# Kernel optimization log

Hardware: AMD Instinct MI355X
Metric: run time of the kernel (lower is better)

## Reference

```python
import jax, jax.numpy as jnp
import numpy as np

B, DIM, IN_DIM, H, W = 4, 256, 128, 128, 128
DD = IN_DIM // 2          # down_dim = 64
HEADS = 8
BN_EPS = 1e-5


def conv2d(x, w, b=None, pad=0, dil=1):
    y = jax.lax.conv_general_dilated(
        x, w, window_strides=(1, 1),
        padding=[(pad, pad), (pad, pad)],
        rhs_dilation=(dil, dil),
        dimension_numbers=('NCHW', 'OIHW', 'NCHW'))
    if b is not None:
        y = y + b[None, :, None, None]
    return y


def bn_relu(x, s, o):
    # eval-mode BatchNorm2d with running_mean=0, running_var=1
    return jax.nn.relu(x * (s / np.sqrt(1.0 + BN_EPS))[None, :, None, None] + o[None, :, None, None])


def setup_inputs() -> dict:
    ks = iter(jax.random.split(jax.random.key(0), 80))

    def w(shape, sc=0.05):
        return sc * jax.random.normal(next(ks), shape, jnp.float32)

    def s(c):
        return 1.0 + 0.1 * jax.random.normal(next(ks), (c,), jnp.float32)

    def o(c):
        return 0.02 * jax.random.normal(next(ks), (c,), jnp.float32)

    d = {}
    d['x'] = jax.random.normal(next(ks), (B, DIM, H, W), jnp.float32)
    d['w_dc'] = w((IN_DIM, DIM, 3, 3)); d['b_dc'] = w((IN_DIM,)); d['s_dc'] = s(IN_DIM); d['o_dc'] = o(IN_DIM)
    d['w1'] = w((DD, IN_DIM, 1, 1)); d['b1'] = w((DD,)); d['s1'] = s(DD); d['o1'] = o(DD)
    d['w2'] = w((DD, DD, 3, 3)); d['b2'] = w((DD,)); d['s2'] = s(DD); d['o2'] = o(DD)
    d['w3'] = w((DD, DD, 3, 3)); d['b3'] = w((DD,)); d['s3'] = s(DD); d['o3'] = o(DD)
    d['w4'] = w((DD, DD, 3, 3)); d['b4'] = w((DD,)); d['s4'] = s(DD); d['o4'] = o(DD)
    d['w5'] = w((DD, IN_DIM, 1, 1)); d['b5'] = w((DD,)); d['s5'] = s(DD); d['o5'] = o(DD)
    d['temperature'] = jnp.ones((HEADS, 1, 1), jnp.float32)
    d['w_po'] = w((DD, 2 * DD, 1, 1))  # project_out, bias=False
    d['w_wa'] = w((DD // 16, DD, 1, 1)); d['b_wa'] = w((DD // 16,)); d['s_wa'] = s(DD // 16); d['o_wa'] = o(DD // 16)
    d['w_wb'] = w((DD, DD // 16, 1, 1)); d['b_wb'] = w((DD,))
    d['w_f'] = w((DD, 5 * DD, 1, 1)); d['b_f'] = w((DD,)); d['s_f'] = s(DD); d['o_f'] = o(DD)
    d['w_oa'] = w((DD // 2, DD, 3, 3)); d['b_oa'] = w((DD // 2,)); d['s_oa'] = s(DD // 2); d['o_oa'] = o(DD // 2)
    d['w_ob'] = w((1, DD // 2, 1, 1)); d['b_ob'] = w((1,))
    return d


def reference(x, w_dc, b_dc, s_dc, o_dc, w1, b1, s1, o1, w2, b2, s2, o2,
              w3, b3, s3, o3, w4, b4, s4, o4, w5, b5, s5, o5,
              temperature, w_po, w_wa, b_wa, s_wa, o_wa, w_wb, b_wb,
              w_f, b_f, s_f, o_f, w_oa, b_oa, s_oa, o_oa, w_ob, b_ob):

    def branch(c):
        b, ch, h, wd = c.shape
        f = jnp.fft.fft2(c)                                   # [b,ch,h,w] complex64 (q=k=v=tepqkv)
        qkv = f.reshape(b, HEADS, ch // HEADS, h * wd)        # v (unnormalized)
        n = jnp.sqrt(jnp.sum(jnp.square(jnp.abs(qkv)), axis=-1, keepdims=True))
        qn = qkv / jnp.maximum(n, 1e-12)                      # F.normalize(dim=-1); q == k
        attn = jnp.einsum('bhcn,bhdn->bhcd', qn, qn) * temperature
        # custom complex normalization: separate real/imag softmax
        attn = jax.lax.complex(jax.nn.softmax(attn.real, axis=-1),
                               jax.nn.softmax(attn.imag, axis=-1))
        of = jnp.abs(jnp.fft.ifft2(jnp.einsum('bhcd,bhdn->bhcn', attn, qkv)))  # ifft2 over (c, hw)
        of = of.reshape(b, ch, h, wd)
        g = jax.nn.sigmoid(conv2d(bn_relu(conv2d(f.real, w_wa, b_wa), s_wa, o_wa), w_wb, b_wb))
        ol = jnp.abs(jnp.fft.ifft2(g * f))                    # ifft2 over (h, w)
        return conv2d(jnp.concatenate([of, ol], axis=1), w_po) + c

    xd = bn_relu(conv2d(x, w_dc, b_dc, pad=1), s_dc, o_dc)
    c1 = bn_relu(conv2d(xd, w1, b1), s1, o1)
    c2 = bn_relu(conv2d(c1, w2, b2, pad=3, dil=3), s2, o2)
    F2 = branch(c2)
    c3 = bn_relu(conv2d(c1 + F2, w3, b3, pad=5, dil=5), s3, o3)
    F3 = branch(c3)
    c4 = bn_relu(conv2d(c1 + F3, w4, b4, pad=7, dil=7), s4, o4)
    F4 = branch(c4)
    # conv5: global avg pool -> 1x1 conv -> bilinear upsample of a 1x1 map == broadcast
    c5 = bn_relu(conv2d(jnp.mean(xd, axis=(2, 3), keepdims=True), w5, b5), s5, o5)
    c5 = jnp.broadcast_to(c5, (c5.shape[0], c5.shape[1], xd.shape[2], xd.shape[3]))
    fused = bn_relu(conv2d(jnp.concatenate([c1, F2, F3, F4, c5], axis=1), w_f, b_f), s_f, o_f)
    return conv2d(bn_relu(conv2d(fused, w_oa, b_oa, pad=1), s_oa, o_oa), w_ob, b_ob)
```

## Files before the change

### kernel.cpp

```cpp
#include <hip/hip_runtime.h>

#define S 16384
#define PI_F 3.14159265358979f

struct Ptrs { const float* p[43]; };

enum : int {
  O_SBDC=0, O_SB1=256, O_SB2=512, O_SB3=768, O_SB4=1024, O_SB5=1280,
  O_SBWA=1536, O_SBF=1792, O_SBOA=2048,
  O_M=2304, O_C5=2816, O_NRM=3072, O_GRAM=3328, O_ATT2=7424, O_BEFF=11520,
  O_WB=16384,
  O_PART=147456,
  O_H=180224,
  O_WP=442368,
  O_A=524288,
  O_FIN=8912896,
  O_CC=25690112,
  O_DRE=29884416, O_DIMG=34078720,
  O_ERE=38273024, O_EIM=42467328,
  O_G=46661632
};

typedef short bfrag __attribute__((ext_vector_type(8)));
typedef float ffrag __attribute__((ext_vector_type(4)));

__device__ __forceinline__ float bf2f(unsigned short u){
  union { unsigned int i; float f; } v; v.i = ((unsigned int)u) << 16; return v.f;
}
__device__ __forceinline__ unsigned short f2bf(float f){
  unsigned int x = __float_as_uint(f);
  unsigned int r = x + 0x7fffu + ((x >> 16) & 1u);
  return (unsigned short)(r >> 16);
}

__global__ void prep_sb_kernel(Ptrs P, float* ws){
  const float r = rsqrtf(1.0f + 1e-5f);
  int bi=0, si=0, oi=0, C=0, dst=0;
  switch (blockIdx.x){
    case 0: bi=2; si=3; oi=4; C=128; dst=O_SBDC; break;
    case 1: bi=6; si=7; oi=8; C=64; dst=O_SB1; break;
    case 2: bi=10; si=11; oi=12; C=64; dst=O_SB2; break;
    case 3: bi=14; si=15; oi=16; C=64; dst=O_SB3; break;
    case 4: bi=18; si=19; oi=20; C=64; dst=O_SB4; break;
    case 5: bi=22; si=23; oi=24; C=64; dst=O_SB5; break;
    case 6: bi=28; si=29; oi=30; C=4;  dst=O_SBWA; break;
    case 7: bi=34; si=35; oi=36; C=64; dst=O_SBF; break;
    default: bi=38; si=39; oi=40; C=32; dst=O_SBOA; break;
  }
  for (int c = threadIdx.x; c < C; c += 256){
    float bb = P.p[bi][c], ss = P.p[si][c], oo = P.p[oi][c];
    float sc = ss * r;
    ws[dst + c] = sc;
    ws[dst + C + c] = bb * sc + oo;
  }
}

__global__ __launch_bounds__(256) void xpad_kernel(const float* __restrict__ x,
    unsigned short* __restrict__ XT){
  int yy = blockIdx.x, b = blockIdx.y;
  long obase = ((long)(b*130) + yy) * (130L*256);
  int tid = threadIdx.x;
  if (yy == 0 || yy == 129){
    uint4 z; z.x=0; z.y=0; z.z=0; z.w=0;
    for (int i = tid; i < 130*256/8; i += 256)
      *(uint4*)(XT + obase + (long)i*8) = z;
    return;
  }
  __shared__ float LT[64][129];
  int y = yy - 1;
  for (int c0 = 0; c0 < 256; c0 += 64){
    for (int idx = tid; idx < 64*128; idx += 256){
      int ci = idx >> 7, xx = idx & 127;
      LT[ci][xx] = x[((long)(b*256 + c0 + ci)*128 + y)*128 + xx];
    }
    __syncthreads();
    for (int idx = tid; idx < 128*16; idx += 256){
      int xp = idx >> 4, c4 = (idx & 15)*4;
      ushort4 v;
      v.x = f2bf(LT[c4][xp]);   v.y = f2bf(LT[c4+1][xp]);
      v.z = f2bf(LT[c4+2][xp]); v.w = f2bf(LT[c4+3][xp]);
      *(ushort4*)(XT + obase + (long)(xp+1)*256 + c0 + c4) = v;
    }
    __syncthreads();
  }
  if (tid < 64){
    ushort4 z; z.x=0; z.y=0; z.z=0; z.w=0;
    *(ushort4*)(XT + obase + tid*4) = z;
    *(ushort4*)(XT + obase + 129L*256 + tid*4) = z;
  }
}

__global__ void wt_kernel(const float* __restrict__ w, unsigned short* __restrict__ WH,
    unsigned short* __restrict__ WL){
  for (int e = blockIdx.x*256 + threadIdx.x; e < 294912; e += gridDim.x*256){
    int c32 = e & 31, co = (e >> 5) & 127, kc = (e >> 12) & 7, sh = e >> 15;
    int ky = sh / 3, kx = sh - ky*3;
    int ci = kc*32 + c32;
    float v = w[((long)(co*256 + ci)*3 + ky)*3 + kx];
    unsigned short h = f2bf(v);
    WH[e] = h;
    WL[e] = f2bf(v - bf2f(h));
  }
}

__global__ void wtg_kernel(Ptrs P, unsigned short* __restrict__ WB){
  const float* w; int cout; long off;
  switch (blockIdx.y){
    case 0: w = P.p[9];  cout = 64; off = 0;      break;
    case 1: w = P.p[13]; cout = 64; off = 73728;  break;
    case 2: w = P.p[17]; cout = 64; off = 147456; break;
    default: w = P.p[37]; cout = 32; off = 221184; break;
  }
  int total = 576*cout;
  unsigned short* WH = WB + off;
  unsigned short* WL = WH + total;
  for (int e = blockIdx.x*256 + threadIdx.x; e < total; e += gridDim.x*256){
    int c32 = e & 31;
    int co = (e >> 5) & (cout - 1);
    int kc = (e / (32*cout)) & 1;
    int sh = e / (64*cout);
    int ky = sh/3, kx = sh - ky*3;
    int ci = kc*32 + c32;
    float v = w[((long)(co*64 + ci)*3 + ky)*3 + kx];
    unsigned short h = f2bf(v);
    WH[e] = h;
    WL[e] = f2bf(v - bf2f(h));
  }
}

__global__ void wtp_kernel(Ptrs P, unsigned short* __restrict__ WP){
  const float* w; int KC, wstr; long off;
  switch (blockIdx.y){
    case 0: w = P.p[5];  KC = 4; wstr = 128; off = 0;     break;
    case 1: w = P.p[26]; KC = 4; wstr = 128; off = 16384; break;
    default: w = P.p[33]; KC = 8; wstr = 320; off = 32768; break;
  }
  int total = KC*64*32;
  unsigned short* WH = WP + off;
  unsigned short* WL = WH + total;
  for (int e = blockIdx.x*256 + threadIdx.x; e < total; e += gridDim.x*256){
    int c32 = e & 31, co = (e >> 5) & 63, kc = e >> 11;
    float v = w[(long)co*wstr + kc*32 + c32];
    unsigned short h = f2bf(v);
    WH[e] = h;
    WL[e] = f2bf(v - bf2f(h));
  }
}

template<int DIL, int BF16IN>
__global__ __launch_bounds__(256) void xpad64_kernel(const void* __restrict__ in1,
    const void* __restrict__ in2, long in_bs, unsigned short* __restrict__ XP){
  constexpr int TW = 128 + 2*DIL;
  int yy = blockIdx.x, b = blockIdx.y;
  long obase = (long)(b*TW + yy) * TW * 64;
  int tid = threadIdx.x;
  if (yy < DIL || yy >= 128 + DIL){
    uint4 z; z.x=0; z.y=0; z.z=0; z.w=0;
    for (int i = tid; i < TW*8; i += 256)
      *(uint4*)(XP + obase + (long)i*8) = z;
    return;
  }
  __shared__ float LT[64][129];
  int y = yy - DIL;
  if (BF16IN){
    const unsigned short* p1 = (const unsigned short*)in1 + (long)b*in_bs + (long)y*128;
    const unsigned short* p2 = in2 ? (const unsigned short*)in2 + (long)b*in_bs + (long)y*128 : nullptr;
    for (int idx = tid; idx < 64*64; idx += 256){
      int ci = idx >> 6, x2 = (idx & 63)*2;
      ushort2 u1 = *(const ushort2*)(p1 + (long)ci*S + x2);
      float a0 = bf2f(u1.x), a1 = bf2f(u1.y);
      if (p2){
        ushort2 u2 = *(const ushort2*)(p2 + (long)ci*S + x2);
        a0 += bf2f(u2.x); a1 += bf2f(u2.y);
      }
      LT[ci][x2] = a0; LT[ci][x2+1] = a1;
    }
  } else {
    const float* p1 = (const float*)in1 + (long)b*in_bs + (long)y*128;
    for (int idx = tid; idx < 64*128; idx += 256){
      int ci = idx >> 7, xx = idx & 127;
      LT[ci][xx] = p1[(long)ci*S + xx];
    }
  }
  __syncthreads();
  for (int i = tid; i < 2*DIL*16; i += 256){
    int side = i / (DIL*16);
    int r = i - side*(DIL*16);
    int xcol = side ? (128 + DIL + (r >> 4)) : (r >> 4);
    ushort4 z; z.x=0; z.y=0; z.z=0; z.w=0;
    *(ushort4*)(XP + obase + (long)xcol*64 + (r & 15)*4) = z;
  }
  for (int idx = tid; idx < 128*16; idx += 256){
    int xp = idx >> 4, c4 = (idx & 15)*4;
    ushort4 v;
    v.x = f2bf(LT[c4][xp]);   v.y = f2bf(LT[c4+1][xp]);
    v.z = f2bf(LT[c4+2][xp]); v.w = f2bf(LT[c4+3][xp]);
    *(ushort4*)(XP + obase + (long)(xp + DIL)*64 + c4) = v;
  }
}

template<int DIL, int KC, int NBLK, int BF16OUT>
__global__ __launch_bounds__(256) void conv3x3_mfma_kernel(
    const unsigned short* __restrict__ XP,
    const unsigned short* __restrict__ WH, const unsigned short* __restrict__ WL,
    const float* __restrict__ scbi, void* __restrict__ out){
  constexpr int CIN = KC*32;
  constexpr int TW = 128 + 2*DIL;
  constexpr int NJ = NBLK/32;
  constexpr int LDA = 36;
  constexpr int NSTG = (TW + 63)/64;
  constexpr int NS = 3*KC;
  __shared__ unsigned short As[2][TW*LDA];
  int bid = blockIdx.x;
  int y = (bid & 7)*16 + ((bid >> 3) & 15);
  int b = (bid >> 7) & 3;
  int n2 = bid >> 9;
  int nb = gridDim.x >> 9; if (nb == 0) nb = 1;
  int coutTotal = nb * NBLK;
  int tid = threadIdx.x, wv = tid >> 6, lane = tid & 63;
  int mhalf = wv & 1, nhalf = wv >> 1;
  int px0 = mhalf*64;
  ffrag acc[4][NJ];
  #pragma unroll
  for (int i = 0; i < 4; i++)
    #pragma unroll
    for (int j = 0; j < NJ; j++)
      #pragma unroll
      for (int r = 0; r < 4; r++) acc[i][j][r] = 0.f;

  int kq = (lane >> 4)*8, rown = lane & 15;
  int sx = tid >> 2, sq = tid & 3;
  int cobase = n2*NBLK + nhalf*(NBLK/2);

  {
    long rowbase = ((long)(b*TW + y))*TW*CIN + sq*8;
    #pragma unroll
    for (int t = 0; t < NSTG; t++){
      int x = sx + 64*t;
      int xc = x < TW ? x : TW - 1;
      uint4 v = *(const uint4*)(XP + rowbase + (long)xc*CIN);
      if (x < TW) *(uint4*)&As[0][x*LDA + sq*8] = v;
    }
  }
  __syncthreads();

  for (int s = 0; s < NS; s++){
    int cur = s & 1;
    int ky = s / KC, kc = s - ky*KC;
    int s2 = (s + 1 < NS) ? s + 1 : s;
    int ky2 = s2 / KC, kc2 = s2 - ky2*KC;
    uint4 pre[NSTG];
    {
      long rowbase = ((long)(b*TW + y + ky2*DIL))*TW*CIN + kc2*32 + sq*8;
      #pragma unroll
      for (int t = 0; t < NSTG; t++){
        int x = sx + 64*t;
        int xc = x < TW ? x : TW - 1;
        pre[t] = *(const uint4*)(XP + rowbase + (long)xc*CIN);
      }
    }
    #pragma unroll
    for (int kx = 0; kx < 3; kx++){
      int step = (ky*3 + kx)*KC + kc;
      bfrag bhf[NJ], blf[NJ];
      #pragma unroll
      for (int j = 0; j < NJ; j++){
        long wb = ((long)step*coutTotal + cobase + j*16 + rown)*32 + kq;
        bhf[j] = *(const bfrag*)(WH + wb);
        blf[j] = *(const bfrag*)(WL + wb);
      }
      bfrag af[4];
      #pragma unroll
      for (int i = 0; i < 4; i++){
        int x = px0 + i*16 + rown + kx*DIL;
        af[i] = *(const bfrag*)&As[cur][x*LDA + kq];
      }
      #pragma unroll
      for (int i = 0; i < 4; i++)
        #pragma unroll
        for (int j = 0; j < NJ; j++){
          acc[i][j] = __builtin_amdgcn_mfma_f32_16x16x32_bf16(af[i], blf[j], acc[i][j], 0, 0, 0);
          acc[i][j] = __builtin_amdgcn_mfma_f32_16x16x32_bf16(af[i], bhf[j], acc[i][j], 0, 0, 0);
        }
    }
    #pragma unroll
    for (int t = 0; t < NSTG; t++){
      int x = sx + 64*t;
      if (x < TW) *(uint4*)&As[cur ^ 1][x*LDA + sq*8] = pre[t];
    }
    __syncthreads();
  }
  #pragma unroll
  for (int i = 0; i < 4; i++){
    int pixel = px0 + i*16 + (lane >> 4)*4;
    #pragma unroll
    for (int j = 0; j < NJ; j++){
      int co = cobase + j*16 + (lane & 15);
      float sc = scbi[co], bb = scbi[coutTotal + co];
      long ooff = ((long)(b*coutTotal + co))*S + y*128 + pixel;
      if (BF16OUT){
        ushort4 w;
        w.x = f2bf(fmaxf(acc[i][j][0]*sc + bb, 0.f));
        w.y = f2bf(fmaxf(acc[i][j][1]*sc + bb, 0.f));
        w.z = f2bf(fmaxf(acc[i][j][2]*sc + bb, 0.f));
        w.w = f2bf(fmaxf(acc[i][j][3]*sc + bb, 0.f));
        *(ushort4*)((unsigned short*)out + ooff) = w;
      } else {
        float* op = (float*)out + ooff;
        #pragma unroll
        for (int r = 0; r < 4; r++)
          op[r] = fmaxf(acc[i][j][r]*sc + bb, 0.f);
      }
    }
  }
}

template<int MODE, int KC, int BF16IN, int BF16OUT>
__global__ __launch_bounds__(256) void conv1x1_mfma_kernel(
    const void* __restrict__ inv, long in_bs,
    const unsigned short* __restrict__ WH, const unsigned short* __restrict__ WL,
    const float* __restrict__ scbi, const float* __restrict__ beff,
    const unsigned short* __restrict__ res, long res_bs,
    void* __restrict__ outv, long out_bs){
  constexpr int LDA = 36;
  __shared__ unsigned short Als[128*LDA];
  __shared__ unsigned short BHs[64*LDA];
  __shared__ unsigned short BLs[64*LDA];
  int bid = blockIdx.x;
  int y = (bid & 7)*16 + ((bid >> 3) & 15);
  int b = bid >> 7;
  int tid = threadIdx.x, wv = tid >> 6, lane = tid & 63;
  int mt0 = (wv & 1)*4, nt0 = (wv >> 1)*2;
  ffrag acc[4][2];
  #pragma unroll
  for (int i = 0; i < 4; i++)
    #pragma unroll
    for (int j = 0; j < 2; j++)
      #pragma unroll
      for (int r = 0; r < 4; r++) acc[i][j][r] = 0.f;
  int pq = tid & 31, cg = tid >> 5;
  int kq = (lane >> 4)*8, rown = lane & 15;
  int wrB = (tid >> 2)*LDA + (tid & 3)*8;
  const float* ibf = (const float*)inv + (long)b*in_bs + y*128;
  const unsigned short* ibs = (const unsigned short*)inv + (long)b*in_bs + y*128;
  unsigned short a[16];
  uint4 BHr, BLr;
  #pragma unroll
  for (int cc = 0; cc < 4; cc++)
    #pragma unroll
    for (int i = 0; i < 4; i++){
      if (BF16IN) a[cc*4 + i] = ibs[(long)(cg*4 + cc)*S + pq + 32*i];
      else        a[cc*4 + i] = f2bf(ibf[(long)(cg*4 + cc)*S + pq + 32*i]);
    }
  BHr = *(const uint4*)(WH + tid*8);
  BLr = *(const uint4*)(WL + tid*8);
  for (int kc = 0; kc < KC; kc++){
    __syncthreads();
    #pragma unroll
    for (int i = 0; i < 4; i++){
      ushort4 v;
      v.x = a[0 + i];  v.y = a[4 + i];
      v.z = a[8 + i];  v.w = a[12 + i];
      *(ushort4*)&Als[(pq + 32*i)*LDA + cg*4] = v;
    }
    *(uint4*)&BHs[wrB] = BHr;
    *(uint4*)&BLs[wrB] = BLr;
    __syncthreads();
    if (kc + 1 < KC){
      #pragma unroll
      for (int cc = 0; cc < 4; cc++)
        #pragma unroll
        for (int i = 0; i < 4; i++){
          long off = (long)((kc + 1)*32 + cg*4 + cc)*S + pq + 32*i;
          if (BF16IN) a[cc*4 + i] = ibs[off];
          else        a[cc*4 + i] = f2bf(ibf[off]);
        }
      long gw = (long)(kc + 1)*2048;
      BHr = *(const uint4*)(WH + gw + tid*8);
      BLr = *(const uint4*)(WL + gw + tid*8);
    }
    bfrag af[4], bhf[2], blf[2];
    #pragma unroll
    for (int i = 0; i < 4; i++)
      af[i] = *(const bfrag*)&Als[((mt0 + i)*16 + rown)*LDA + kq];
    #pragma unroll
    for (int j = 0; j < 2; j++){
      bhf[j] = *(const bfrag*)&BHs[((nt0 + j)*16 + rown)*LDA + kq];
      blf[j] = *(const bfrag*)&BLs[((nt0 + j)*16 + rown)*LDA + kq];
    }
    #pragma unroll
    for (int i = 0; i < 4; i++)
      #pragma unroll
      for (int j = 0; j < 2; j++){
        acc[i][j] = __builtin_amdgcn_mfma_f32_16x16x32_bf16(af[i], blf[j], acc[i][j], 0, 0, 0);
        acc[i][j] = __builtin_amdgcn_mfma_f32_16x16x32_bf16(af[i], bhf[j], acc[i][j], 0, 0, 0);
      }
  }
  #pragma unroll
  for (int i = 0; i < 4; i++){
    int pixel = (mt0 + i)*16 + (lane >> 4)*4;
    #pragma unroll
    for (int j = 0; j < 2; j++){
      int co = (nt0 + j)*16 + (lane & 15);
      long ooff = (long)b*out_bs + (long)co*S + y*128 + pixel;
      float vv[4];
      if (MODE == 1){
        ushort4 rv = *(const ushort4*)(res + (long)b*res_bs + (long)co*S + y*128 + pixel);
        vv[0] = acc[i][j][0] + bf2f(rv.x);
        vv[1] = acc[i][j][1] + bf2f(rv.y);
        vv[2] = acc[i][j][2] + bf2f(rv.z);
        vv[3] = acc[i][j][3] + bf2f(rv.w);
      } else if (MODE == 0){
        #pragma unroll
        for (int r = 0; r < 4; r++)
          vv[r] = fmaxf(acc[i][j][r]*scbi[co] + scbi[64 + co], 0.f);
      } else {
        #pragma unroll
        for (int r = 0; r < 4; r++)
          vv[r] = fmaxf(acc[i][j][r]*scbi[co] + beff[b*64 + co], 0.f);
      }
      if (BF16OUT){
        ushort4 w;
        w.x = f2bf(vv[0]); w.y = f2bf(vv[1]); w.z = f2bf(vv[2]); w.w = f2bf(vv[3]);
        *(ushort4*)((unsigned short*)outv + ooff) = w;
      } else {
        float* op = (float*)outv + ooff;
        #pragma unroll
        for (int r = 0; r < 4; r++) op[r] = vv[r];
      }
    }
  }
}

__device__ __forceinline__ void fft128_mk_tw(float (&tws)[8], float (&twc)[8],
                                             float sign, int lane){
  float a0 = sign * (2.0f*PI_F/128.0f) * (float)lane;
  __sincosf(a0, &tws[0], &twc[0]);
  int i = 1;
  #pragma unroll
  for (int h = 32; h >= 1; h >>= 1, i++){
    int j = lane & (h - 1);
    float a = sign * (2.0f*PI_F/128.0f) * (float)(j * (64/h));
    __sincosf(a, &tws[i], &twc[i]);
  }
}

__device__ __forceinline__ void fft128(float& z0r, float& z0i, float& z1r, float& z1i,
    const float (&tws)[8], const float (&twc)[8], int lane){
  {
    float ar = z0r, ai = z0i, br = z1r, bi = z1i;
    z0r = ar + br; z0i = ai + bi;
    float dr = ar - br, di = ai - bi;
    float s = tws[0], c = twc[0];
    z1r = dr*c - di*s; z1i = dr*s + di*c;
  }
  int idx = 1;
  #pragma unroll
  for (int h = 32; h >= 1; h >>= 1, idx++){
    float s = tws[idx], c = twc[idx];
    bool up = (lane & h) != 0;
    float pr, pi, nr, ni;
    pr = __shfl_xor(z0r, h, 64); pi = __shfl_xor(z0i, h, 64);
    if (!up){ nr = z0r + pr; ni = z0i + pi; }
    else { float dr = pr - z0r, di = pi - z0i; nr = dr*c - di*s; ni = dr*s + di*c; }
    z0r = nr; z0i = ni;
    pr = __shfl_xor(z1r, h, 64); pi = __shfl_xor(z1i, h, 64);
    if (!up){ nr = z1r + pr; ni = z1i + pi; }
    else { float dr = pr - z1r, di = pi - z1i; nr = dr*c - di*s; ni = dr*s + di*c; }
    z1r = nr; z1i = ni;
  }
}


__global__ __launch_bounds__(1024) void fft2_fwd_kernel(const unsigned short* __restrict__ in,
    unsigned short* __restrict__ outRe, unsigned short* __restrict__ outIm){
  __shared__ float lre[128][129];
  __shared__ float lim[128][129];
  int plane = blockIdx.x;
  int tid = threadIdx.x, wv = tid >> 6, lane = tid & 63;
  long pbase = (long)plane * S;
  for (int i = tid; i < S/4; i += 1024){
    int px = i*4; int r = px >> 7, c = px & 127;
    ushort4 v = *(const ushort4*)(in + pbase + px);
    lre[r][c] = bf2f(v.x); lre[r][c+1] = bf2f(v.y);
    lre[r][c+2] = bf2f(v.z); lre[r][c+3] = bf2f(v.w);
  }
  float tws[8], twc[8];
  fft128_mk_tw(tws, twc, -1.0f, lane);
  __syncthreads();
  #pragma unroll
  for (int rr = 0; rr < 8; rr++){
    int r = wv*8 + rr;
    float z0r = lre[r][lane], z0i = 0.f;
    float z1r = lre[r][lane + 64], z1i = 0.f;
    fft128(z0r, z0i, z1r, z1i, tws, twc, lane);
    int k = __brev(lane) >> 25;
    lre[r][k] = z0r;     lim[r][k] = z0i;
    lre[r][k+1] = z1r;   lim[r][k+1] = z1i;
  }
  __syncthreads();
  #pragma unroll
  for (int cc = 0; cc < 8; cc++){
    int c = wv*8 + cc;
    float z0r = lre[lane][c], z0i = lim[lane][c];
    float z1r = lre[lane + 64][c], z1i = lim[lane + 64][c];
    fft128(z0r, z0i, z1r, z1i, tws, twc, lane);
    int k = __brev(lane) >> 25;
    lre[k][c] = z0r;     lim[k][c] = z0i;
    lre[k+1][c] = z1r;   lim[k+1][c] = z1i;
  }
  __syncthreads();
  for (int i = tid; i < S/2; i += 1024){
    int px = i*2; int r = px >> 7, c = px & 127;
    ushort2 vr, vi;
    vr.x = f2bf(lre[r][c]); vr.y = f2bf(lre[r][c+1]);
    vi.x = f2bf(lim[r][c]); vi.y = f2bf(lim[r][c+1]);
    *(ushort2*)(outRe + pbase + px) = vr;
    *(ushort2*)(outIm + pbase + px) = vi;
  }
}

__global__ __launch_bounds__(1024) void ifft2_gate_abs_ol_kernel(
    const unsigned short* __restrict__ Dre, const unsigned short* __restrict__ Dim,
    const float* __restrict__ H, const float* __restrict__ wb, const float* __restrict__ bwb,
    unsigned short* __restrict__ AB){
  __shared__ float lre[128][129];
  __shared__ float lim[128][129];
  int plane = blockIdx.x;
  int b = plane >> 6, ch = plane & 63;
  int tid = threadIdx.x, wv = tid >> 6, lane = tid & 63;
  long pbase = (long)plane * S;
  float w0 = wb[ch*4], w1 = wb[ch*4+1], w2 = wb[ch*4+2], w3 = wb[ch*4+3];
  float bw = bwb[ch];
  const float* Hb = H + (long)b*4*S;
  for (int i = tid; i < S/2; i += 1024){
    int px = i*2;
    float2 h0 = *(const float2*)(Hb + px);
    float2 h1 = *(const float2*)(Hb + S + px);
    float2 h2 = *(const float2*)(Hb + 2*S + px);
    float2 h3 = *(const float2*)(Hb + 3*S + px);
    ushort2 ur = *(const ushort2*)(Dre + pbase + px);
    ushort2 ui = *(const ushort2*)(Dim + pbase + px);
    float hva = bw + w0*h0.x + w1*h1.x + w2*h2.x + w3*h3.x;
    float hvb = bw + w0*h0.y + w1*h1.y + w2*h2.y + w3*h3.y;
    float ga = 1.0f / (1.0f + __expf(-hva));
    float gb = 1.0f / (1.0f + __expf(-hvb));
    int r = px >> 7, c = px & 127;
    lre[r][c]   = bf2f(ur.x) * ga;  lim[r][c]   = bf2f(ui.x) * ga;
    lre[r][c+1] = bf2f(ur.y) * gb;  lim[r][c+1] = bf2f(ui.y) * gb;
  }
  float tws[8], twc[8];
  fft128_mk_tw(tws, twc, 1.0f, lane);
  __syncthreads();
  #pragma unroll
  for (int cc = 0; cc < 8; cc++){
    int c = wv*8 + cc;
    float z0r = lre[lane][c], z0i = lim[lane][c];
    float z1r = lre[lane + 64][c], z1i = lim[lane + 64][c];
    fft128(z0r, z0i, z1r, z1i, tws, twc, lane);
    int k = __brev(lane) >> 25;
    lre[k][c] = z0r;     lim[k][c] = z0i;
    lre[k+1][c] = z1r;   lim[k+1][c] = z1i;
  }
  __syncthreads();
  unsigned short* out = AB + ((long)(b*128 + 64 + ch)) * S;
  #pragma unroll
  for (int rr = 0; rr < 8; rr++){
    int r = wv*8 + rr;
    float z0r = lre[r][lane], z0i = lim[r][lane];
    float z1r = lre[r][lane + 64], z1i = lim[r][lane + 64];
    fft128(z0r, z0i, z1r, z1i, tws, twc, lane);
    int k = __brev(lane) >> 25;
    ushort2 v;
    v.x = f2bf(sqrtf(z0r*z0r + z0i*z0i) * (1.0f/16384.0f));
    v.y = f2bf(sqrtf(z1r*z1r + z1i*z1i) * (1.0f/16384.0f));
    *(ushort2*)(out + (long)r*128 + k) = v;
  }
}

__global__ __launch_bounds__(1024) void ifft2_attn_abs_ofT_kernel(
    const unsigned short* __restrict__ Dre, const unsigned short* __restrict__ Dim,
    const float* __restrict__ ATT2, unsigned short* __restrict__ AB){
  __shared__ float lre[128][129];
  __shared__ float lim[128][129];
  int plane = blockIdx.x;
  int b = plane >> 6, ch = plane & 63;
  int bh = plane >> 3;
  int cp = plane & 7;
  int tid = threadIdx.x, wv = tid >> 6, lane = tid & 63;
  long hbase = (long)bh * 8 * S;
  float wr[8], wi[8];
  #pragma unroll
  for (int d = 0; d < 8; d++){
    wr[d] = ATT2[bh*128 + (cp*8 + d)*2];
    wi[d] = ATT2[bh*128 + (cp*8 + d)*2 + 1];
  }
  for (int i = tid; i < S/4; i += 1024){
    int px = i*4;
    float sr0=0.f, si0=0.f, sr1=0.f, si1=0.f, sr2=0.f, si2=0.f, sr3=0.f, si3=0.f;
    #pragma unroll
    for (int d = 0; d < 8; d++){
      ushort4 ur = *(const ushort4*)(Dre + hbase + (long)d*S + px);
      ushort4 ui = *(const ushort4*)(Dim + hbase + (long)d*S + px);
      float xr0 = bf2f(ur.x), xi0 = bf2f(ui.x);
      float xr1 = bf2f(ur.y), xi1 = bf2f(ui.y);
      float xr2 = bf2f(ur.z), xi2 = bf2f(ui.z);
      float xr3 = bf2f(ur.w), xi3 = bf2f(ui.w);
      sr0 += wr[d]*xr0 - wi[d]*xi0;  si0 += wr[d]*xi0 + wi[d]*xr0;
      sr1 += wr[d]*xr1 - wi[d]*xi1;  si1 += wr[d]*xi1 + wi[d]*xr1;
      sr2 += wr[d]*xr2 - wi[d]*xi2;  si2 += wr[d]*xi2 + wi[d]*xr2;
      sr3 += wr[d]*xr3 - wi[d]*xi3;  si3 += wr[d]*xi3 + wi[d]*xr3;
    }
    int r = px >> 7, c = px & 127;
    lre[r][c]   = sr0;  lim[r][c]   = si0;
    lre[r][c+1] = sr1;  lim[r][c+1] = si1;
    lre[r][c+2] = sr2;  lim[r][c+2] = si2;
    lre[r][c+3] = sr3;  lim[r][c+3] = si3;
  }
  float tws[8], twc[8];
  fft128_mk_tw(tws, twc, 1.0f, lane);
  __syncthreads();
  #pragma unroll
  for (int cc = 0; cc < 8; cc++){
    int c = wv*8 + cc;
    float z0r = lre[lane][c], z0i = lim[lane][c];
    float z1r = lre[lane + 64][c], z1i = lim[lane + 64][c];
    fft128(z0r, z0i, z1r, z1i, tws, twc, lane);
    int k = __brev(lane) >> 25;
    float s, co;
    float a0 = (2.0f*PI_F/16384.0f) * (float)(c * k);
    __sincosf(a0, &s, &co);
    float t = z0r*co - z0i*s; z0i = z0r*s + z0i*co; z0r = t;
    float a1 = (2.0f*PI_F/16384.0f) * (float)(c * (k + 1));
    __sincosf(a1, &s, &co);
    t = z1r*co - z1i*s; z1i = z1r*s + z1i*co; z1r = t;
    lre[k][c] = z0r;     lim[k][c] = z0i;
    lre[k+1][c] = z1r;   lim[k+1][c] = z1i;
  }
  __syncthreads();
  float absv[8][2];
  #pragma unroll
  for (int rr = 0; rr < 8; rr++){
    int r = wv*8 + rr;
    float z0r = lre[r][lane], z0i = lim[r][lane];
    float z1r = lre[r][lane + 64], z1i = lim[r][lane + 64];
    fft128(z0r, z0i, z1r, z1i, tws, twc, lane);
    absv[rr][0] = sqrtf(z0r*z0r + z0i*z0i) * (1.0f/16384.0f);
    absv[rr][1] = sqrtf(z1r*z1r + z1i*z1i) * (1.0f/16384.0f);
  }
  __syncthreads();
  int k2 = __brev(lane) >> 25;
  #pragma unroll
  for (int rr = 0; rr < 8; rr++){
    int r = wv*8 + rr;
    lre[k2][r] = absv[rr][0];
    lre[k2+1][r] = absv[rr][1];
  }
  __syncthreads();
  unsigned short* out = AB + ((long)(b*128 + ch)) * S;
  for (int i = tid; i < S/2; i += 1024){
    int px = i*2; int r = px >> 7, c = px & 127;
    ushort2 v;
    v.x = f2bf(lre[r][c]); v.y = f2bf(lre[r][c+1]);
    *(ushort2*)(out + px) = v;
  }
}

__global__ __launch_bounds__(256) void gram_part_kernel(
    const unsigned short* __restrict__ Dre, const unsigned short* __restrict__ Dim,
    float* __restrict__ PART){
  int bh = blockIdx.x, slab = blockIdx.y;
  long base = (long)bh * 8 * S;
  int n0 = slab * 2048;
  float accr[36], acci[36], nsq[8];
  #pragma unroll
  for (int i = 0; i < 36; i++){ accr[i] = 0.f; acci[i] = 0.f; }
  #pragma unroll
  for (int i = 0; i < 8; i++) nsq[i] = 0.f;
  for (int it = 0; it < 4; it++){
    int n = n0 + (it*256 + threadIdx.x)*2;
    float xr[8][2], xi[8][2];
    #pragma unroll
    for (int c = 0; c < 8; c++){
      ushort2 ur = *(const ushort2*)(Dre + base + (long)c*S + n);
      ushort2 ui = *(const ushort2*)(Dim + base + (long)c*S + n);
      xr[c][0] = bf2f(ur.x); xr[c][1] = bf2f(ur.y);
      xi[c][0] = bf2f(ui.x); xi[c][1] = bf2f(ui.y);
      nsq[c] += xr[c][0]*xr[c][0] + xi[c][0]*xi[c][0]
              + xr[c][1]*xr[c][1] + xi[c][1]*xi[c][1];
    }
    int t = 0;
    #pragma unroll
    for (int c = 0; c < 8; c++)
      #pragma unroll
      for (int d = c; d < 8; d++){
        accr[t] += xr[c][0]*xr[d][0] - xi[c][0]*xi[d][0]
                 + xr[c][1]*xr[d][1] - xi[c][1]*xi[d][1];
        acci[t] += xr[c][0]*xi[d][0] + xi[c][0]*xr[d][0]
                 + xr[c][1]*xi[d][1] + xi[c][1]*xr[d][1];
        t++;
      }
  }
  __shared__ float red[4][80];
  int wv = threadIdx.x >> 6, lane = threadIdx.x & 63;
  #pragma unroll
  for (int i = 0; i < 80; i++){
    float v = (i < 36) ? accr[i] : (i < 72) ? acci[i - 36] : nsq[i - 72];
    #pragma unroll
    for (int o = 32; o; o >>= 1) v += __shfl_xor(v, o, 64);
    if (lane == 0) red[wv][i] = v;
  }
  __syncthreads();
  if (threadIdx.x < 80){
    int i = threadIdx.x;
    PART[(long)(bh*8 + slab)*80 + i] = red[0][i] + red[1][i] + red[2][i] + red[3][i];
  }
}

__global__ void attn2f_kernel(const float* __restrict__ PART,
    const float* __restrict__ temp, float* __restrict__ ATT2){
  __shared__ float ssum[80];
  __shared__ float sar[64], sai[64];
  int bh = blockIdx.x;
  int t = threadIdx.x;
  if (t < 80){
    float s = 0.f;
    for (int i = 0; i < 8; i++) s += PART[(long)(bh*8 + i)*80 + t];
    ssum[t] = s;
  }
  __syncthreads();
  if (t >= 64) return;
  int lane = t;
  int c = lane >> 3, d = lane & 7;
  int lo = min(c, d), hi = max(c, d);
  int t2 = lo*8 - lo*(lo - 1)/2 + (hi - lo);
  float nnc = fmaxf(sqrtf(ssum[72 + c]), 1e-12f);
  float nnd = fmaxf(sqrtf(ssum[72 + d]), 1e-12f);
  float inv = temp[bh & 7] / (nnc * nnd);
  float ar = ssum[t2] * inv, ai = ssum[36 + t2] * inv;
  float m = ar;
  m = fmaxf(m, __shfl_xor(m, 1, 64)); m = fmaxf(m, __shfl_xor(m, 2, 64)); m = fmaxf(m, __shfl_xor(m, 4, 64));
  float e = __expf(ar - m);
  float su = e;
  su += __shfl_xor(su, 1, 64); su += __shfl_xor(su, 2, 64); su += __shfl_xor(su, 4, 64);
  ar = e / su;
  m = ai;
  m = fmaxf(m, __shfl_xor(m, 1, 64)); m = fmaxf(m, __shfl_xor(m, 2, 64)); m = fmaxf(m, __shfl_xor(m, 4, 64));
  e = __expf(ai - m);
  su = e;
  su += __shfl_xor(su, 1, 64); su += __shfl_xor(su, 2, 64); su += __shfl_xor(su, 4, 64);
  ai = e / su;
  sar[lane] = ar; sai[lane] = ai;
  __syncthreads();
  const float ct[8] = {1.f, 0.70710678f, 0.f, -0.70710678f, -1.f, -0.70710678f, 0.f, 0.70710678f};
  const float st[8] = {0.f, 0.70710678f, 1.f, 0.70710678f, 0.f, -0.70710678f, -1.f, -0.70710678f};
  int cp = c;
  float sr = 0.f, si = 0.f;
  #pragma unroll
  for (int cc = 0; cc < 8; cc++){
    int k = (cc * cp) & 7;
    float a = sar[cc*8 + d], b2 = sai[cc*8 + d];
    sr += ct[k]*a - st[k]*b2;
    si += ct[k]*b2 + st[k]*a;
  }
  float2 v; v.x = sr * 0.125f; v.y = si * 0.125f;
  ((float2*)ATT2)[bh*64 + lane] = v;
}

__global__ __launch_bounds__(256) void gateh_kernel(const unsigned short* __restrict__ Dre,
    const float* __restrict__ wa, const float* __restrict__ sbwa, float* __restrict__ H){
  int b = blockIdx.y;
  int px = blockIdx.x*256 + threadIdx.x;
  long base = (long)b * 64 * S + px;
  float h0 = 0.f, h1 = 0.f, h2 = 0.f, h3 = 0.f;
  for (int ci = 0; ci < 64; ci++){
    float x = bf2f(Dre[base + (long)ci*S]);
    h0 += wa[ci]*x; h1 += wa[64 + ci]*x; h2 += wa[128 + ci]*x; h3 += wa[192 + ci]*x;
  }
  long ob = (long)b * 4 * S + px;
  H[ob]       = fmaxf(h0*sbwa[0] + sbwa[4], 0.f);
  H[ob + S]   = fmaxf(h1*sbwa[1] + sbwa[5], 0.f);
  H[ob + 2*S] = fmaxf(h2*sbwa[2] + sbwa[6], 0.f);
  H[ob + 3*S] = fmaxf(h3*sbwa[3] + sbwa[7], 0.f);
}

__global__ __launch_bounds__(256) void mean_kernel(const float* __restrict__ A, float* __restrict__ M){
  int p = blockIdx.x;
  long base = (long)p * S;
  float s = 0.f;
  for (int n = threadIdx.x; n < S; n += 256) s += A[base + n];
  #pragma unroll
  for (int o = 32; o; o >>= 1) s += __shfl_xor(s, o, 64);
  __shared__ float sm[4];
  if ((threadIdx.x & 63) == 0) sm[threadIdx.x >> 6] = s;
  __syncthreads();
  if (threadIdx.x == 0) M[p] = (sm[0] + sm[1] + sm[2] + sm[3]) * (1.0f/16384.0f);
}

__global__ void c5beff_kernel(const float* __restrict__ W5, const float* __restrict__ sb5,
    const float* __restrict__ WF, const float* __restrict__ sbf,
    const float* __restrict__ M, float* __restrict__ BEFF){
  __shared__ float c5s[256];
  int t = threadIdx.x;
  if (t >= 256) return;
  int b = t >> 6, co = t & 63;
  float s = 0.f;
  for (int ci = 0; ci < 128; ci++) s += W5[co*128 + ci] * M[b*128 + ci];
  c5s[t] = fmaxf(s * sb5[co] + sb5[64 + co], 0.f);
  __syncthreads();
  float s2 = 0.f;
  for (int j = 0; j < 64; j++) s2 += WF[co*320 + 256 + j] * c5s[b*64 + j];
  BEFF[t] = s2 * sbf[co] + sbf[64 + co];
}

__global__ __launch_bounds__(256) void ob_kernel(const float* __restrict__ Tin,
    const float* __restrict__ wob, const float* __restrict__ bob, float* __restrict__ out){
  int b = blockIdx.y;
  int px = blockIdx.x*1024 + (threadIdx.x & 63)*4 + (threadIdx.x >> 6)*256;
  float b0 = bob[0];
  float4 a; a.x = b0; a.y = b0; a.z = b0; a.w = b0;
  for (int ci = 0; ci < 32; ci++){
    float4 v = *(const float4*)(Tin + ((long)b*32 + ci)*S + px);
    float w = wob[ci];
    a.x += w*v.x; a.y += w*v.y; a.z += w*v.z; a.w += w*v.w;
  }
  *(float4*)(out + (long)b*S + px) = a;
}

extern "C" void kernel_launch(void* const* d_in, const int* in_sizes, int n_in,
                              void* d_out, int out_size, void* d_ws, size_t ws_size,
                              hipStream_t stream){
  float* ws = (float*)d_ws;
  Ptrs P;
  for (int i = 0; i < 43 && i < n_in; i++) P.p[i] = (const float*)d_in[i];
  float* out = (float*)d_out;

  float* A   = ws + O_A;
  float* CC  = ws + O_CC;
  float* G   = ws + O_G;
  float* H   = ws + O_H;

  unsigned short* FINB = (unsigned short*)(ws + O_FIN);
  unsigned short* CCB  = (unsigned short*)(ws + O_CC);
  unsigned short* DRE16 = (unsigned short*)(ws + O_DRE);
  unsigned short* DIM16 = (unsigned short*)(ws + O_DIMG);
  unsigned short* AB    = (unsigned short*)(ws + O_A);

  unsigned short* XT  = (unsigned short*)(ws + O_DRE);
  unsigned short* WHd = (unsigned short*)(ws + O_CC);
  unsigned short* WLd = (unsigned short*)(ws + O_CC + 147456);
  unsigned short* WB  = (unsigned short*)(ws + O_WB);
  unsigned short* WP  = (unsigned short*)(ws + O_WP);
  unsigned short* XP  = (unsigned short*)(ws + O_ERE);

  prep_sb_kernel<<<dim3(9), dim3(256), 0, stream>>>(P, ws);
  xpad_kernel<<<dim3(130, 4), dim3(256), 0, stream>>>(P.p[0], XT);
  wt_kernel<<<dim3(128), dim3(256), 0, stream>>>(P.p[1], WHd, WLd);
  wtg_kernel<<<dim3(16, 4), dim3(256), 0, stream>>>(P, WB);
  wtp_kernel<<<dim3(8, 3), dim3(256), 0, stream>>>(P, WP);

  conv3x3_mfma_kernel<1,8,64,0><<<dim3(1024), dim3(256), 0, stream>>>(
      XT, WHd, WLd, ws + O_SBDC, A);

  mean_kernel<<<dim3(512), dim3(256), 0, stream>>>(A, ws + O_M);
  c5beff_kernel<<<dim3(1), dim3(256), 0, stream>>>(
      P.p[21], ws + O_SB5, P.p[33], ws + O_SBF, ws + O_M, ws + O_BEFF);

  conv1x1_mfma_kernel<0,4,0,1><<<dim3(512), dim3(256), 0, stream>>>(
      A, 128*S, WP, WP + 8192, ws + O_SB1, nullptr, nullptr, 0, FINB, 256*S);

  for (int k = 0; k < 3; k++){
    const float* sb = ws + (k == 0 ? O_SB2 : k == 1 ? O_SB3 : O_SB4);
    const unsigned short* in2 = (k == 0) ? nullptr : FINB + (long)(64*k)*S;
    unsigned short* wh = WB + (k == 0 ? 0 : k == 1 ? 73728 : 147456);
    if (k == 0){
      xpad64_kernel<3,1><<<dim3(134, 4), dim3(256), 0, stream>>>(FINB, in2, 256*S, XP);
      conv3x3_mfma_kernel<3,2,64,1><<<dim3(512), dim3(256), 0, stream>>>(
          XP, wh, wh + 36864, sb, CCB);
    } else if (k == 1){
      xpad64_kernel<5,1><<<dim3(138, 4), dim3(256), 0, stream>>>(FINB, in2, 256*S, XP);
      conv3x3_mfma_kernel<5,2,64,1><<<dim3(512), dim3(256), 0, stream>>>(
          XP, wh, wh + 36864, sb, CCB);
    } else {
      xpad64_kernel<7,1><<<dim3(142, 4), dim3(256), 0, stream>>>(FINB, in2, 256*S, XP);
      conv3x3_mfma_kernel<7,2,64,1><<<dim3(512), dim3(256), 0, stream>>>(
          XP, wh, wh + 36864, sb, CCB);
    }

    fft2_fwd_kernel<<<dim3(256), dim3(1024), 0, stream>>>(CCB, DRE16, DIM16);
    gram_part_kernel<<<dim3(32, 8), dim3(256), 0, stream>>>(DRE16, DIM16, ws + O_PART);
    attn2f_kernel<<<dim3(32), dim3(128), 0, stream>>>(ws + O_PART, P.p[25], ws + O_ATT2);
    gateh_kernel<<<dim3(64, 4), dim3(256), 0, stream>>>(DRE16, P.p[27], ws + O_SBWA, H);
    ifft2_gate_abs_ol_kernel<<<dim3(256), dim3(1024), 0, stream>>>(
        DRE16, DIM16, H, P.p[31], P.p[32], AB);
    ifft2_attn_abs_ofT_kernel<<<dim3(256), dim3(1024), 0, stream>>>(
        DRE16, DIM16, ws + O_ATT2, AB);
    conv1x1_mfma_kernel<1,4,1,1><<<dim3(512), dim3(256), 0, stream>>>(
        AB, 128*S, WP + 16384, WP + 24576, nullptr, nullptr, CCB, 64*S,
        FINB + (long)(64*(k + 1))*S, 256*S);
  }

  conv1x1_mfma_kernel<2,8,1,0><<<dim3(512), dim3(256), 0, stream>>>(
      FINB, 256*S, WP + 32768, WP + 49152, ws + O_SBF, ws + O_BEFF, nullptr, 0, CC, 64*S);
  xpad64_kernel<1,0><<<dim3(130, 4), dim3(256), 0, stream>>>(CC, nullptr, 64*S, XP);
  conv3x3_mfma_kernel<1,2,32,0><<<dim3(512), dim3(256), 0, stream>>>(
      XP, WB + 221184, WB + 221184 + 18432, ws + O_SBOA, G);
  ob_kernel<<<dim3(16, 4), dim3(256), 0, stream>>>(G, P.p[41], P.p[42], out);
}
```

Measured before the change: 895.1 us.

## Split first 3x3 conv over input channels and fuse BN-ReLU into consumers

Replaces the first 256→128 3x3 conv with a split-K kernel that runs twice as many blocks, each covering half the input channels, and writes two bf16 partial sums. The BN+ReLU epilogue moves into the mean kernel and into a new 1x1-conv input mode that adds both partials and applies the activation while loading. This aims to raise parallelism and to cut the fp32 intermediate traffic to bf16. It costs an extra partial-sum round trip, and both partials are rounded to bf16 before being summed. The gate kernel is also changed to handle two pixels per thread with vector loads and half the grid.

```diff
diff --git a/kernel.cpp b/kernel.cpp
--- a/kernel.cpp
+++ b/kernel.cpp
@@ -20,6 +20,7 @@
   O_ERE=38273024, O_EIM=42467328,
   O_G=46661632
 };
+#define APSTRIDE 8388608L
 
 typedef short bfrag __attribute__((ext_vector_type(8)));
 typedef float ffrag __attribute__((ext_vector_type(4)));
@@ -196,6 +197,103 @@
     v.x = f2bf(LT[c4][xp]);   v.y = f2bf(LT[c4+1][xp]);
     v.z = f2bf(LT[c4+2][xp]); v.w = f2bf(LT[c4+3][xp]);
     *(ushort4*)(XP + obase + (long)(xp + DIL)*64 + c4) = v;
+  }
+}
+
+__global__ __launch_bounds__(256) void convdc_split_kernel(
+    const unsigned short* __restrict__ XP,
+    const unsigned short* __restrict__ WH, const unsigned short* __restrict__ WL,
+    unsigned short* __restrict__ out){
+  constexpr int CIN = 256, TW = 130, LDA = 36, NSTG = 3;
+  __shared__ unsigned short As[2][TW*LDA];
+  int bid = blockIdx.x;
+  int y = (bid & 7)*16 + ((bid >> 3) & 15);
+  int b = (bid >> 7) & 3;
+  int n2 = (bid >> 9) & 1;
+  int ks = bid >> 10;
+  int tid = threadIdx.x, wv = tid >> 6, lane = tid & 63;
+  int mhalf = wv & 1, nhalf = wv >> 1;
+  int px0 = mhalf*64;
+  ffrag acc[4][2];
+  #pragma unroll
+  for (int i = 0; i < 4; i++)
+    #pragma unroll
+    for (int j = 0; j < 2; j++)
+      #pragma unroll
+      for (int r = 0; r < 4; r++) acc[i][j][r] = 0.f;
+  int kq = (lane >> 4)*8, rown = lane & 15;
+  int sx = tid >> 2, sq = tid & 3;
+  int cobase = n2*64 + nhalf*32;
+  {
+    long rowbase = ((long)(b*TW + y))*TW*CIN + (ks*4)*32 + sq*8;
+    #pragma unroll
+    for (int t = 0; t < NSTG; t++){
+      int x = sx + 64*t;
+      int xc = x < TW ? x : TW - 1;
+      uint4 v = *(const uint4*)(XP + rowbase + (long)xc*CIN);
+      if (x < TW) *(uint4*)&As[0][x*LDA + sq*8] = v;
+    }
+  }
+  __syncthreads();
+  for (int s = 0; s < 12; s++){
+    int cur = s & 1;
+    int ky = s >> 2, kcl = s & 3;
+    int kc = ks*4 + kcl;
+    int s2 = (s + 1 < 12) ? s + 1 : s;
+    int ky2 = s2 >> 2, kc2 = ks*4 + (s2 & 3);
+    uint4 pre[NSTG];
+    {
+      long rowbase = ((long)(b*TW + y + ky2))*TW*CIN + kc2*32 + sq*8;
+      #pragma unroll
+      for (int t = 0; t < NSTG; t++){
+        int x = sx + 64*t;
+        int xc = x < TW ? x : TW - 1;
+        pre[t] = *(const uint4*)(XP + rowbase + (long)xc*CIN);
+      }
+    }
+    #pragma unroll
+    for (int kx = 0; kx < 3; kx++){
+      int step = (ky*3 + kx)*8 + kc;
+      bfrag bhf[2], blf[2];
+      #pragma unroll
+      for (int j = 0; j < 2; j++){
+        long wb = ((long)step*128 + cobase + j*16 + rown)*32 + kq;
+        bhf[j] = *(const bfrag*)(WH + wb);
+        blf[j] = *(const bfrag*)(WL + wb);
+      }
+      bfrag af[4];
+      #pragma unroll
+      for (int i = 0; i < 4; i++){
+        int x = px0 + i*16 + rown + kx;
+        af[i] = *(const bfrag*)&As[cur][x*LDA + kq];
+      }
+      #pragma unroll
+      for (int i = 0; i < 4; i++)
+        #pragma unroll
+        for (int j = 0; j < 2; j++){
+          acc[i][j] = __builtin_amdgcn_mfma_f32_16x16x32_bf16(af[i], blf[j], acc[i][j], 0, 0, 0);
+          acc[i][j] = __builtin_amdgcn_mfma_f32_16x16x32_bf16(af[i], bhf[j], acc[i][j], 0, 0, 0);
+        }
+    }
+    #pragma unroll
+    for (int t = 0; t < NSTG; t++){
+      int x = sx + 64*t;
+      if (x < TW) *(uint4*)&As[cur ^ 1][x*LDA + sq*8] = pre[t];
+    }
+    __syncthreads();
+  }
+  unsigned short* dst = out + ks*APSTRIDE;
+  #pragma unroll
+  for (int i = 0; i < 4; i++){
+    int pixel = px0 + i*16 + (lane >> 4)*4;
+    #pragma unroll
+    for (int j = 0; j < 2; j++){
+      int co = cobase + j*16 + (lane & 15);
+      ushort4 w;
+      w.x = f2bf(acc[i][j][0]); w.y = f2bf(acc[i][j][1]);
+      w.z = f2bf(acc[i][j][2]); w.w = f2bf(acc[i][j][3]);
+      *(ushort4*)(dst + ((long)(b*128 + co))*S + y*128 + pixel) = w;
+    }
   }
 }
 
@@ -349,8 +447,13 @@
   for (int cc = 0; cc < 4; cc++)
     #pragma unroll
     for (int i = 0; i < 4; i++){
-      if (BF16IN) a[cc*4 + i] = ibs[(long)(cg*4 + cc)*S + pq + 32*i];
-      else        a[cc*4 + i] = f2bf(ibf[(long)(cg*4 + cc)*S + pq + 32*i]);
+      long off = (long)(cg*4 + cc)*S + pq + 32*i;
+      if (BF16IN == 1) a[cc*4 + i] = ibs[off];
+      else if (BF16IN == 2){
+        float v = bf2f(ibs[off]) + bf2f(ibs[off + APSTRIDE]);
+        int ci = cg*4 + cc;
+        a[cc*4 + i] = f2bf(fmaxf(v*beff[ci] + beff[128 + ci], 0.f));
+      } else a[cc*4 + i] = f2bf(ibf[off]);
     }
   BHr = *(const uint4*)(WH + tid*8);
   BLr = *(const uint4*)(WL + tid*8);
@@ -372,8 +475,12 @@
         #pragma unroll
         for (int i = 0; i < 4; i++){
           long off = (long)((kc + 1)*32 + cg*4 + cc)*S + pq + 32*i;
-          if (BF16IN) a[cc*4 + i] = ibs[off];
-          else        a[cc*4 + i] = f2bf(ibf[off]);
+          if (BF16IN == 1) a[cc*4 + i] = ibs[off];
+          else if (BF16IN == 2){
+            float v = bf2f(ibs[off]) + bf2f(ibs[off + APSTRIDE]);
+            int ci = (kc + 1)*32 + cg*4 + cc;
+            a[cc*4 + i] = f2bf(fmaxf(v*beff[ci] + beff[128 + ci], 0.f));
+          } else a[cc*4 + i] = f2bf(ibf[off]);
         }
       long gw = (long)(kc + 1)*2048;
       BHr = *(const uint4*)(WH + gw + tid*8);
@@ -770,25 +877,42 @@
 __global__ __launch_bounds__(256) void gateh_kernel(const unsigned short* __restrict__ Dre,
     const float* __restrict__ wa, const float* __restrict__ sbwa, float* __restrict__ H){
   int b = blockIdx.y;
-  int px = blockIdx.x*256 + threadIdx.x;
+  int px = (blockIdx.x*256 + threadIdx.x)*2;
   long base = (long)b * 64 * S + px;
-  float h0 = 0.f, h1 = 0.f, h2 = 0.f, h3 = 0.f;
+  float h0a = 0.f, h1a = 0.f, h2a = 0.f, h3a = 0.f;
+  float h0b = 0.f, h1b = 0.f, h2b = 0.f, h3b = 0.f;
   for (int ci = 0; ci < 64; ci++){
-    float x = bf2f(Dre[base + (long)ci*S]);
-    h0 += wa[ci]*x; h1 += wa[64 + ci]*x; h2 += wa[128 + ci]*x; h3 += wa[192 + ci]*x;
+    ushort2 u = *(const ushort2*)(Dre + base + (long)ci*S);
+    float xa = bf2f(u.x), xb = bf2f(u.y);
+    float w0 = wa[ci], w1 = wa[64 + ci], w2 = wa[128 + ci], w3 = wa[192 + ci];
+    h0a += w0*xa; h1a += w1*xa; h2a += w2*xa; h3a += w3*xa;
+    h0b += w0*xb; h1b += w1*xb; h2b += w2*xb; h3b += w3*xb;
   }
   long ob = (long)b * 4 * S + px;
-  H[ob]       = fmaxf(h0*sbwa[0] + sbwa[4], 0.f);
-  H[ob + S]   = fmaxf(h1*sbwa[1] + sbwa[5], 0.f);
-  H[ob + 2*S] = fmaxf(h2*sbwa[2] + sbwa[6], 0.f);
-  H[ob + 3*S] = fmaxf(h3*sbwa[3] + sbwa[7], 0.f);
-}
-
-__global__ __launch_bounds__(256) void mean_kernel(const float* __restrict__ A, float* __restrict__ M){
+  float2 v;
+  v.x = fmaxf(h0a*sbwa[0] + sbwa[4], 0.f); v.y = fmaxf(h0b*sbwa[0] + sbwa[4], 0.f);
+  *(float2*)(H + ob) = v;
+  v.x = fmaxf(h1a*sbwa[1] + sbwa[5], 0.f); v.y = fmaxf(h1b*sbwa[1] + sbwa[5], 0.f);
+  *(float2*)(H + ob + S) = v;
+  v.x = fmaxf(h2a*sbwa[2] + sbwa[6], 0.f); v.y = fmaxf(h2b*sbwa[2] + sbwa[6], 0.f);
+  *(float2*)(H + ob + 2*S) = v;
+  v.x = fmaxf(h3a*sbwa[3] + sbwa[7], 0.f); v.y = fmaxf(h3b*sbwa[3] + sbwa[7], 0.f);
+  *(float2*)(H + ob + 3*S) = v;
+}
+
+__global__ __launch_bounds__(256) void mean2_kernel(const unsigned short* __restrict__ P0,
+    const float* __restrict__ sbdc, float* __restrict__ M){
   int p = blockIdx.x;
+  int ci = p & 127;
+  float sc = sbdc[ci], bb = sbdc[128 + ci];
   long base = (long)p * S;
   float s = 0.f;
-  for (int n = threadIdx.x; n < S; n += 256) s += A[base + n];
+  for (int n = threadIdx.x*2; n < S; n += 512){
+    ushort2 a0 = *(const ushort2*)(P0 + base + n);
+    ushort2 a1 = *(const ushort2*)(P0 + APSTRIDE + base + n);
+    s += fmaxf((bf2f(a0.x) + bf2f(a1.x))*sc + bb, 0.f)
+       + fmaxf((bf2f(a0.y) + bf2f(a1.y))*sc + bb, 0.f);
+  }
   #pragma unroll
   for (int o = 32; o; o >>= 1) s += __shfl_xor(s, o, 64);
   __shared__ float sm[4];
@@ -835,11 +959,11 @@
   for (int i = 0; i < 43 && i < n_in; i++) P.p[i] = (const float*)d_in[i];
   float* out = (float*)d_out;
 
-  float* A   = ws + O_A;
   float* CC  = ws + O_CC;
   float* G   = ws + O_G;
   float* H   = ws + O_H;
 
+  unsigned short* AP0 = (unsigned short*)(ws + O_A);
   unsigned short* FINB = (unsigned short*)(ws + O_FIN);
   unsigned short* CCB  = (unsigned short*)(ws + O_CC);
   unsigned short* DRE16 = (unsigned short*)(ws + O_DRE);
@@ -859,15 +983,14 @@
   wtg_kernel<<<dim3(16, 4), dim3(256), 0, stream>>>(P, WB);
   wtp_kernel<<<dim3(8, 3), dim3(256), 0, stream>>>(P, WP);
 
-  conv3x3_mfma_kernel<1,8,64,0><<<dim3(1024), dim3(256), 0, stream>>>(
-      XT, WHd, WLd, ws + O_SBDC, A);
-
-  mean_kernel<<<dim3(512), dim3(256), 0, stream>>>(A, ws + O_M);
+  convdc_split_kernel<<<dim3(2048), dim3(256), 0, stream>>>(XT, WHd, WLd, AP0);
+
+  mean2_kernel<<<dim3(512), dim3(256), 0, stream>>>(AP0, ws + O_SBDC, ws + O_M);
   c5beff_kernel<<<dim3(1), dim3(256), 0, stream>>>(
       P.p[21], ws + O_SB5, P.p[33], ws + O_SBF, ws + O_M, ws + O_BEFF);
 
-  conv1x1_mfma_kernel<0,4,0,1><<<dim3(512), dim3(256), 0, stream>>>(
-      A, 128*S, WP, WP + 8192, ws + O_SB1, nullptr, nullptr, 0, FINB, 256*S);
+  conv1x1_mfma_kernel<0,4,2,1><<<dim3(512), dim3(256), 0, stream>>>(
+      AP0, 128*S, WP, WP + 8192, ws + O_SB1, ws + O_SBDC, nullptr, 0, FINB, 256*S);
 
   for (int k = 0; k < 3; k++){
     const float* sb = ws + (k == 0 ? O_SB2 : k == 1 ? O_SB3 : O_SB4);
@@ -890,7 +1013,7 @@
     fft2_fwd_kernel<<<dim3(256), dim3(1024), 0, stream>>>(CCB, DRE16, DIM16);
     gram_part_kernel<<<dim3(32, 8), dim3(256), 0, stream>>>(DRE16, DIM16, ws + O_PART);
     attn2f_kernel<<<dim3(32), dim3(128), 0, stream>>>(ws + O_PART, P.p[25], ws + O_ATT2);
-    gateh_kernel<<<dim3(64, 4), dim3(256), 0, stream>>>(DRE16, P.p[27], ws + O_SBWA, H);
+    gateh_kernel<<<dim3(32, 4), dim3(256), 0, stream>>>(DRE16, P.p[27], ws + O_SBWA, H);
     ifft2_gate_abs_ol_kernel<<<dim3(256), dim3(1024), 0, stream>>>(
         DRE16, DIM16, H, P.p[31], P.p[32], AB);
     ifft2_attn_abs_ofT_kernel<<<dim3(256), dim3(1024), 0, stream>>>(
```

Result: no change. 894.7 us (-0.0%).
